# Performance work log

Measured on AMD Instinct MI355X. Metric: run time of the kernel, lower is better.

The kernel has to match this reference:

```python
import jax, jax.numpy as jnp
import numpy as np

N_NODES = 16384
IN_DIM = 256
HEADS = 2
OUT_CH = 256  # per head
SLOPE = 0.2


def _gat_conv(x, edge_index, W, att_src, att_dst, bias):
    """PyG GATConv (v1), heads=2, concat=True, add_self_loops=True."""
    N = x.shape[0]
    loop = jnp.arange(N)
    src = jnp.concatenate([edge_index[0], loop])  # message sources j
    dst = jnp.concatenate([edge_index[1], loop])  # message targets i
    h = (x @ W.T).reshape(N, HEADS, OUT_CH)          # [N,H,C]
    a_src = (h * att_src).sum(-1)                    # [N,H]
    a_dst = (h * att_dst).sum(-1)                    # [N,H]
    e = jax.nn.leaky_relu(a_src[src] + a_dst[dst], SLOPE)  # [E,H]
    # segment softmax over incoming edges of each dst node
    m = jax.ops.segment_max(e, dst, num_segments=N)
    e = jnp.exp(e - m[dst])
    s = jax.ops.segment_sum(e, dst, num_segments=N)
    alpha = e / s[dst]                               # [E,H]
    out = jax.ops.segment_sum(alpha[:, :, None] * h[src], dst, num_segments=N)
    return out.reshape(N, HEADS * OUT_CH) + bias


def _safe_cdist(x):
    sq = (x * x).sum(-1)
    d2 = sq[:, None] + sq[None, :] - 2.0 * (x @ x.T)
    d2 = jnp.maximum(d2, 0.0)
    d = jnp.sqrt(jnp.where(d2 > 0, d2, 1.0))
    return jnp.where(d2 > 0, d, 0.0)


def _linear_init(k, out_f, in_f):
    b = 1.0 / np.sqrt(in_f)
    k1, k2 = jax.random.split(k)
    W = jax.random.uniform(k1, (out_f, in_f), minval=-b, maxval=b, dtype=jnp.float32)
    bias = jax.random.uniform(k2, (out_f,), minval=-b, maxval=b, dtype=jnp.float32)
    return W, bias


def setup_inputs() -> dict:
    key = jax.random.key(0)
    ks = jax.random.split(key, 12)
    x = jax.random.normal(ks[0], (N_NODES, IN_DIM), dtype=jnp.float32)
    edge_index = jax.random.randint(ks[1], (2, 524288), 0, N_NODES, dtype=jnp.int64)
    g = 1.0 / np.sqrt(IN_DIM)
    conv_W = jax.random.normal(ks[2], (HEADS * OUT_CH, IN_DIM), dtype=jnp.float32) * g
    att_src = jax.random.normal(ks[3], (HEADS, OUT_CH), dtype=jnp.float32) * g
    att_dst = jax.random.normal(ks[4], (HEADS, OUT_CH), dtype=jnp.float32) * g
    conv_b = jnp.zeros((HEADS * OUT_CH,), dtype=jnp.float32)
    Wa, ba = _linear_init(ks[5], 256, 512)
    W1, b1 = _linear_init(ks[6], 128, 256)
    W2, b2 = _linear_init(ks[7], 64, 128)
    W3, b3 = _linear_init(ks[8], 32, 64)
    W4, b4 = _linear_init(ks[9], 3, 32)
    return {"x": x, "edge_index": edge_index, "conv_W": conv_W,
            "att_src": att_src, "att_dst": att_dst, "conv_b": conv_b,
            "Wa": Wa, "ba": ba, "W1": W1, "b1": b1, "W2": W2, "b2": b2,
            "W3": W3, "b3": b3, "W4": W4, "b4": b4}


def reference(x, edge_index, conv_W, att_src, att_dst, conv_b,
              Wa, ba, W1, b1, W2, b2, W3, b3, W4, b4):
    h = _gat_conv(x, edge_index, conv_W, att_src, att_dst, conv_b)
    h = jax.nn.relu(h)                      # dropout = identity (eval)
    h = jax.nn.relu(h @ Wa.T + ba)
    h = jax.nn.relu(h @ W1.T + b1)
    h = jax.nn.relu(h @ W2.T + b2)
    h = jax.nn.relu(h @ W3.T + b3)
    h = h @ W4.T + b4                        # [N,3]
    return _safe_cdist(h)                    # [N,N]
```

## Files before the change

### kernel.cpp

```cpp
#include <hip/hip_runtime.h>
#include <hip/hip_bf16.h>
#include <math.h>

#define N_NODES 16384
#define E_EDGES 524288
#define E_TOT   (E_EDGES + N_NODES)
#define HDIM    512
#define SLOPE   0.2f

__global__ void detect_kernel(const void* __restrict__ ei, int* __restrict__ flag) {
    int t = threadIdx.x;
    int v = ((const int*)ei)[2 * t + 1];
    unsigned long long b = __ballot(v != 0);
    if (t == 0) *flag = (b == 0ULL) ? 1 : 0;
}

__device__ __forceinline__ int edge_val(const void* ei, int idx, int is64) {
    if (is64) return (int)((const long long*)ei)[idx];
    return ((const int*)ei)[idx];
}

__global__ __launch_bounds__(256) void count_kernel(const void* __restrict__ ei,
                                                    const int* __restrict__ flag,
                                                    int* __restrict__ deg) {
    int e = blockIdx.x * 256 + threadIdx.x;
    if (e >= E_TOT) return;
    int is64 = *flag;
    int dst = (e < E_EDGES) ? edge_val(ei, E_EDGES + e, is64) : (e - E_EDGES);
    atomicAdd(&deg[dst], 1);
}

__global__ __launch_bounds__(1024) void scan_kernel(const int* __restrict__ deg,
                                                    int* __restrict__ rowptr,
                                                    int* __restrict__ cursor) {
    __shared__ int ps[1024];
    int tid = threadIdx.x;
    int base = tid * 16;
    int loc[16];
    int s = 0;
#pragma unroll
    for (int i = 0; i < 16; ++i) { loc[i] = deg[base + i]; s += loc[i]; }
    ps[tid] = s;
    __syncthreads();
    for (int off = 1; off < 1024; off <<= 1) {
        int t = (tid >= off) ? ps[tid - off] : 0;
        __syncthreads();
        if (tid >= off) ps[tid] += t;
        __syncthreads();
    }
    int run = ps[tid] - s;
#pragma unroll
    for (int i = 0; i < 16; ++i) {
        rowptr[base + i] = run;
        cursor[base + i] = run;
        run += loc[i];
    }
    if (tid == 1023) rowptr[N_NODES] = run;
}

__global__ __launch_bounds__(256) void fill_kernel(const void* __restrict__ ei,
                                                   const int* __restrict__ flag,
                                                   int* __restrict__ cursor,
                                                   int* __restrict__ col) {
    int e = blockIdx.x * 256 + threadIdx.x;
    if (e >= E_TOT) return;
    int is64 = *flag;
    int src, dst;
    if (e < E_EDGES) {
        src = edge_val(ei, e, is64);
        dst = edge_val(ei, E_EDGES + e, is64);
    } else {
        src = dst = e - E_EDGES;
    }
    int slot = atomicAdd(&cursor[dst], 1);
    col[slot] = src;
}

template <bool RELU, bool BIAS>
__global__ __launch_bounds__(256) void gemm128(const float* __restrict__ A,
                                               const float* __restrict__ B,
                                               const float* __restrict__ bias,
                                               float* __restrict__ C,
                                               int M, int N, int K) {
    __shared__ float As[16][132];
    __shared__ float Bs[16][132];
    int tid = threadIdx.x;
    int tx = tid & 15, ty = tid >> 4;
    int bm0 = blockIdx.y * 128, bn0 = blockIdx.x * 128;

    float acc[8][8];
#pragma unroll
    for (int i = 0; i < 8; ++i)
#pragma unroll
        for (int j = 0; j < 8; ++j) acc[i][j] = 0.f;

    for (int k0 = 0; k0 < K; k0 += 16) {
        float4 av[2], bv[2];
#pragma unroll
        for (int l = 0; l < 2; ++l) {
            int idx = l * 256 + tid;
            int row = idx >> 2, k4 = idx & 3;
            av[l] = *(const float4*)&A[(size_t)(bm0 + row) * K + k0 + k4 * 4];
            bv[l] = *(const float4*)&B[(size_t)(bn0 + row) * K + k0 + k4 * 4];
        }
        __syncthreads();
#pragma unroll
        for (int l = 0; l < 2; ++l) {
            int idx = l * 256 + tid;
            int row = idx >> 2, k4 = idx & 3;
            As[k4 * 4 + 0][row] = av[l].x;
            As[k4 * 4 + 1][row] = av[l].y;
            As[k4 * 4 + 2][row] = av[l].z;
            As[k4 * 4 + 3][row] = av[l].w;
            Bs[k4 * 4 + 0][row] = bv[l].x;
            Bs[k4 * 4 + 1][row] = bv[l].y;
            Bs[k4 * 4 + 2][row] = bv[l].z;
            Bs[k4 * 4 + 3][row] = bv[l].w;
        }
        __syncthreads();
#pragma unroll
        for (int kk = 0; kk < 16; ++kk) {
            float4 a0 = *(const float4*)&As[kk][ty * 8];
            float4 a1 = *(const float4*)&As[kk][ty * 8 + 4];
            float4 b0 = *(const float4*)&Bs[kk][tx * 8];
            float4 b1 = *(const float4*)&Bs[kk][tx * 8 + 4];
            float a[8] = {a0.x, a0.y, a0.z, a0.w, a1.x, a1.y, a1.z, a1.w};
            float b[8] = {b0.x, b0.y, b0.z, b0.w, b1.x, b1.y, b1.z, b1.w};
#pragma unroll
            for (int i = 0; i < 8; ++i)
#pragma unroll
                for (int j = 0; j < 8; ++j) acc[i][j] = fmaf(a[i], b[j], acc[i][j]);
        }
        __syncthreads();
    }

    float bvv[8];
#pragma unroll
    for (int j = 0; j < 8; ++j) bvv[j] = BIAS ? bias[bn0 + tx * 8 + j] : 0.f;

#pragma unroll
    for (int i = 0; i < 8; ++i) {
        int row = bm0 + ty * 8 + i;
        float v[8];
#pragma unroll
        for (int j = 0; j < 8; ++j) {
            v[j] = acc[i][j] + bvv[j];
            if (RELU) v[j] = fmaxf(v[j], 0.f);
        }
        float* cp = &C[(size_t)row * N + bn0 + tx * 8];
        *(float4*)cp = make_float4(v[0], v[1], v[2], v[3]);
        *(float4*)(cp + 4) = make_float4(v[4], v[5], v[6], v[7]);
    }
}

__global__ __launch_bounds__(256) void attn_kernel(const float* __restrict__ h,
                                                   const float* __restrict__ att_src,
                                                   const float* __restrict__ att_dst,
                                                   float* __restrict__ a_src,
                                                   float* __restrict__ a_dst) {
    int n = blockIdx.x, tid = threadIdx.x;
    float h0 = h[(size_t)n * HDIM + tid];
    float h1 = h[(size_t)n * HDIM + 256 + tid];
    __shared__ float4 red[256];
    red[tid] = make_float4(h0 * att_src[tid], h1 * att_src[256 + tid],
                           h0 * att_dst[tid], h1 * att_dst[256 + tid]);
    __syncthreads();
    for (int off = 128; off > 0; off >>= 1) {
        if (tid < off) {
            float4 o = red[tid + off];
            float4 m = red[tid];
            m.x += o.x; m.y += o.y; m.z += o.z; m.w += o.w;
            red[tid] = m;
        }
        __syncthreads();
    }
    if (tid == 0) {
        float4 r = red[0];
        a_src[2 * n] = r.x; a_src[2 * n + 1] = r.y;
        a_dst[2 * n] = r.z; a_dst[2 * n + 1] = r.w;
    }
}

__device__ __forceinline__ float lrelu(float x) {
    return fmaxf(x, 0.f) + SLOPE * fminf(x, 0.f);
}

__global__ __launch_bounds__(256) void aggregate_kernel(const float* __restrict__ h,
                                                        const float* __restrict__ a_src,
                                                        const float* __restrict__ a_dst,
                                                        const int* __restrict__ rowptr,
                                                        const int* __restrict__ col,
                                                        const float* __restrict__ conv_b,
                                                        float* __restrict__ act0) {
    int n = blockIdx.x, tid = threadIdx.x;
    int rs = rowptr[n], re = rowptr[n + 1];
    float ad0 = a_dst[2 * n], ad1 = a_dst[2 * n + 1];
    __shared__ float r0[256], r1[256];

    float m0 = -1e30f, m1 = -1e30f;
    for (int k = rs + tid; k < re; k += 256) {
        int s = col[k];
        float e0 = lrelu(a_src[2 * s] + ad0);
        float e1 = lrelu(a_src[2 * s + 1] + ad1);
        m0 = fmaxf(m0, e0); m1 = fmaxf(m1, e1);
    }
    r0[tid] = m0; r1[tid] = m1;
    __syncthreads();
    for (int off = 128; off > 0; off >>= 1) {
        if (tid < off) {
            r0[tid] = fmaxf(r0[tid], r0[tid + off]);
            r1[tid] = fmaxf(r1[tid], r1[tid + off]);
        }
        __syncthreads();
    }
    float M0 = r0[0], M1 = r1[0];
    __syncthreads();

    float s0 = 0.f, s1 = 0.f;
    for (int k = rs + tid; k < re; k += 256) {
        int s = col[k];
        float e0 = lrelu(a_src[2 * s] + ad0);
        float e1 = lrelu(a_src[2 * s + 1] + ad1);
        s0 += expf(e0 - M0); s1 += expf(e1 - M1);
    }
    r0[tid] = s0; r1[tid] = s1;
    __syncthreads();
    for (int off = 128; off > 0; off >>= 1) {
        if (tid < off) {
            r0[tid] += r0[tid + off];
            r1[tid] += r1[tid + off];
        }
        __syncthreads();
    }
    float inv0 = 1.f / r0[0], inv1 = 1.f / r1[0];
    __syncthreads();

    __shared__ float al0[256], al1[256];
    __shared__ int sc[256];
    float acc0 = 0.f, acc1 = 0.f;
    for (int base = rs; base < re; base += 256) {
        int len = min(256, re - base);
        if (tid < len) {
            int s = col[base + tid];
            sc[tid] = s;
            float e0 = lrelu(a_src[2 * s] + ad0);
            float e1 = lrelu(a_src[2 * s + 1] + ad1);
            al0[tid] = expf(e0 - M0) * inv0;
            al1[tid] = expf(e1 - M1) * inv1;
        }
        __syncthreads();
        for (int kk = 0; kk < len; ++kk) {
            const float* hr = h + (size_t)sc[kk] * HDIM;
            acc0 = fmaf(al0[kk], hr[tid], acc0);
            acc1 = fmaf(al1[kk], hr[tid + 256], acc1);
        }
        __syncthreads();
    }
    act0[(size_t)n * HDIM + tid] = fmaxf(acc0 + conv_b[tid], 0.f);
    act0[(size_t)n * HDIM + 256 + tid] = fmaxf(acc1 + conv_b[tid + 256], 0.f);
}

__global__ __launch_bounds__(256) void mlp_tail_kernel(const float* __restrict__ act2,
                                                       const float* __restrict__ W2, const float* __restrict__ b2,
                                                       const float* __restrict__ W3, const float* __restrict__ b3,
                                                       const float* __restrict__ W4, const float* __restrict__ b4,
                                                       float* __restrict__ p) {
    __shared__ float w2[64][129];
    __shared__ float w3[32][65];
    __shared__ float w4[3][33];
    __shared__ float bb2[64], bb3[32], bb4[3];
    __shared__ float xb[4][128];
    __shared__ float yb[4][64];
    __shared__ float zb[4][32];
    int tid = threadIdx.x;
    for (int idx = tid; idx < 64 * 128; idx += 256) w2[idx >> 7][idx & 127] = W2[idx];
    for (int idx = tid; idx < 32 * 64; idx += 256) w3[idx >> 6][idx & 63] = W3[idx];
    for (int idx = tid; idx < 96; idx += 256) w4[idx / 32][idx % 32] = W4[idx];
    if (tid < 64) bb2[tid] = b2[tid];
    if (tid < 32) bb3[tid] = b3[tid];
    if (tid < 3) bb4[tid] = b4[tid];
    __syncthreads();

    int n0 = blockIdx.x * 64;
    int nl = tid >> 6, lane = tid & 63;
    for (int g = 0; g < 64; g += 4) {
        for (int l = tid; l < 512; l += 256)
            xb[l >> 7][l & 127] = act2[(size_t)(n0 + g + (l >> 7)) * 128 + (l & 127)];
        __syncthreads();
        float y = bb2[lane];
#pragma unroll 8
        for (int j = 0; j < 128; ++j) y = fmaf(w2[lane][j], xb[nl][j], y);
        yb[nl][lane] = fmaxf(y, 0.f);
        __syncthreads();
        if (lane < 32) {
            float z = bb3[lane];
#pragma unroll 8
            for (int j = 0; j < 64; ++j) z = fmaf(w3[lane][j], yb[nl][j], z);
            zb[nl][lane] = fmaxf(z, 0.f);
        }
        __syncthreads();
        if (lane < 3) {
            float c = bb4[lane];
#pragma unroll
            for (int j = 0; j < 32; ++j) c = fmaf(w4[lane][j], zb[nl][j], c);
            p[(size_t)(n0 + g + nl) * 3 + lane] = c;
        }
        __syncthreads();
    }
}

__global__ __launch_bounds__(256) void cdist_kernel(const float* __restrict__ p,
                                                    float* __restrict__ out) {
    int tid = threadIdx.x;
    int j0 = blockIdx.x * 1024 + tid * 4;
    int i0 = blockIdx.y * 64;
    __shared__ float pi[64][3];
    for (int l = tid; l < 192; l += 256) pi[l / 3][l % 3] = p[i0 * 3 + l];
    float px[4], py[4], pz[4];
#pragma unroll
    for (int q = 0; q < 4; ++q) {
        const float* pp = p + (size_t)(j0 + q) * 3;
        px[q] = pp[0]; py[q] = pp[1]; pz[q] = pp[2];
    }
    __syncthreads();
#pragma unroll 4
    for (int i = 0; i < 64; ++i) {
        float ax = pi[i][0], ay = pi[i][1], az = pi[i][2];
        float o[4];
#pragma unroll
        for (int q = 0; q < 4; ++q) {
            float dx = ax - px[q], dy = ay - py[q], dz = az - pz[q];
            float d2 = fmaf(dx, dx, fmaf(dy, dy, dz * dz));
            o[q] = (d2 > 0.f) ? sqrtf(d2) : 0.f;
        }
        *(float4*)(out + (size_t)(i0 + i) * N_NODES + j0) = make_float4(o[0], o[1], o[2], o[3]);
    }
}

extern "C" void kernel_launch(void* const* d_in, const int* in_sizes, int n_in,
                              void* d_out, int out_size, void* d_ws, size_t ws_size,
                              hipStream_t stream) {
    const float* x       = (const float*)d_in[0];
    const void*  ei      = d_in[1];
    const float* conv_W  = (const float*)d_in[2];
    const float* att_src = (const float*)d_in[3];
    const float* att_dst = (const float*)d_in[4];
    const float* conv_b  = (const float*)d_in[5];
    const float* Wa = (const float*)d_in[6];  const float* ba = (const float*)d_in[7];
    const float* W1 = (const float*)d_in[8];  const float* b1 = (const float*)d_in[9];
    const float* W2 = (const float*)d_in[10]; const float* b2 = (const float*)d_in[11];
    const float* W3 = (const float*)d_in[12]; const float* b3 = (const float*)d_in[13];
    const float* W4 = (const float*)d_in[14]; const float* b4 = (const float*)d_in[15];
    float* out = (float*)d_out;

    float* ws_f  = (float*)d_ws;
    float* h     = ws_f;
    float* act0  = ws_f + (size_t)N_NODES * HDIM;
    float* a_src = act0 + (size_t)N_NODES * HDIM;
    float* a_dst = a_src + N_NODES * 2;
    int* deg     = (int*)(a_dst + N_NODES * 2);
    int* rowptr  = deg + N_NODES;
    int* cursor  = rowptr + N_NODES + 1;
    int* col     = cursor + N_NODES;
    int* flag    = col + E_TOT;
    float* act1  = h;
    float* act2  = h + (size_t)N_NODES * 256;
    float* p3    = act2 + (size_t)N_NODES * 128;

    hipMemsetAsync(deg, 0, N_NODES * sizeof(int), stream);
    detect_kernel<<<1, 64, 0, stream>>>(ei, flag);

    gemm128<false, false><<<dim3(4, 128), 256, 0, stream>>>(x, conv_W, nullptr, h,
                                                            N_NODES, 512, 256);
    attn_kernel<<<N_NODES, 256, 0, stream>>>(h, att_src, att_dst, a_src, a_dst);

    count_kernel<<<E_TOT / 256, 256, 0, stream>>>(ei, flag, deg);
    scan_kernel<<<1, 1024, 0, stream>>>(deg, rowptr, cursor);
    fill_kernel<<<E_TOT / 256, 256, 0, stream>>>(ei, flag, cursor, col);

    aggregate_kernel<<<N_NODES, 256, 0, stream>>>(h, a_src, a_dst, rowptr, col,
                                                  conv_b, act0);

    gemm128<true, true><<<dim3(2, 128), 256, 0, stream>>>(act0, Wa, ba, act1,
                                                          N_NODES, 256, 512);
    gemm128<true, true><<<dim3(1, 128), 256, 0, stream>>>(act1, W1, b1, act2,
                                                          N_NODES, 128, 256);
    mlp_tail_kernel<<<N_NODES / 64, 256, 0, stream>>>(act2, W2, b2, W3, b3, W4, b4, p3);

    cdist_kernel<<<dim3(16, 256), 256, 0, stream>>>(p3, out);
}
```

Before: 1.642 ms.

## Replace FP32 SIMT GEMMs with split-bf16 MFMA GEMMs via hi/lo operand expansion

Each FP32 GEMM operand is split into bf16 high and low parts and laid out as a K-tripled matrix. The A side is stored as [hi, hi, lo] and the B side as [hi, lo, hi], so one bf16 MFMA GEMM over 3K computes hi*hi + hi*lo + lo*hi, which approximates FP32 accuracy. The new GEMM uses global_load_lds direct-to-LDS copies, XOR-swizzled LDS tiles and 16x16x32 bf16 MFMA instructions. This adds split kernels and extra memory traffic for the expanded operands, and the workspace layout is reorganised so act1 and act2 no longer alias h.

```diff
diff --git a/kernel.cpp b/kernel.cpp
--- a/kernel.cpp
+++ b/kernel.cpp
@@ -1,12 +1,28 @@
 #include <hip/hip_runtime.h>
-#include <hip/hip_bf16.h>
 #include <math.h>
+#include <stdint.h>
 
 #define N_NODES 16384
 #define E_EDGES 524288
 #define E_TOT   (E_EDGES + N_NODES)
 #define HDIM    512
 #define SLOPE   0.2f
+
+typedef unsigned short ushort_t;
+typedef __attribute__((ext_vector_type(8))) short short8v;
+typedef __attribute__((ext_vector_type(4))) float f32x4;
+
+__device__ __forceinline__ unsigned short f2bf(float f) {
+    unsigned u = __float_as_uint(f);
+    return (unsigned short)((u + 0x7fffu + ((u >> 16) & 1u)) >> 16);
+}
+__device__ __forceinline__ float bf2f(unsigned short s) {
+    return __uint_as_float(((unsigned)s) << 16);
+}
+
+#define GLOAD_LDS16(G, L)                                                               \
+    __builtin_amdgcn_global_load_lds((const __attribute__((address_space(1))) unsigned int*)(G), \
+                                     (__attribute__((address_space(3))) unsigned int*)(L), 16, 0, 0)
 
 __global__ void detect_kernel(const void* __restrict__ ei, int* __restrict__ flag) {
     int t = threadIdx.x;
@@ -76,80 +92,121 @@
     col[slot] = src;
 }
 
-template <bool RELU, bool BIAS>
-__global__ __launch_bounds__(256) void gemm128(const float* __restrict__ A,
-                                               const float* __restrict__ B,
-                                               const float* __restrict__ bias,
-                                               float* __restrict__ C,
-                                               int M, int N, int K) {
-    __shared__ float As[16][132];
-    __shared__ float Bs[16][132];
-    int tid = threadIdx.x;
-    int tx = tid & 15, ty = tid >> 4;
-    int bm0 = blockIdx.y * 128, bn0 = blockIdx.x * 128;
-
-    float acc[8][8];
-#pragma unroll
-    for (int i = 0; i < 8; ++i)
-#pragma unroll
-        for (int j = 0; j < 8; ++j) acc[i][j] = 0.f;
-
-    for (int k0 = 0; k0 < K; k0 += 16) {
-        float4 av[2], bv[2];
-#pragma unroll
-        for (int l = 0; l < 2; ++l) {
-            int idx = l * 256 + tid;
-            int row = idx >> 2, k4 = idx & 3;
-            av[l] = *(const float4*)&A[(size_t)(bm0 + row) * K + k0 + k4 * 4];
-            bv[l] = *(const float4*)&B[(size_t)(bn0 + row) * K + k0 + k4 * 4];
-        }
-        __syncthreads();
-#pragma unroll
-        for (int l = 0; l < 2; ++l) {
-            int idx = l * 256 + tid;
-            int row = idx >> 2, k4 = idx & 3;
-            As[k4 * 4 + 0][row] = av[l].x;
-            As[k4 * 4 + 1][row] = av[l].y;
-            As[k4 * 4 + 2][row] = av[l].z;
-            As[k4 * 4 + 3][row] = av[l].w;
-            Bs[k4 * 4 + 0][row] = bv[l].x;
-            Bs[k4 * 4 + 1][row] = bv[l].y;
-            Bs[k4 * 4 + 2][row] = bv[l].z;
-            Bs[k4 * 4 + 3][row] = bv[l].w;
-        }
-        __syncthreads();
-#pragma unroll
-        for (int kk = 0; kk < 16; ++kk) {
-            float4 a0 = *(const float4*)&As[kk][ty * 8];
-            float4 a1 = *(const float4*)&As[kk][ty * 8 + 4];
-            float4 b0 = *(const float4*)&Bs[kk][tx * 8];
-            float4 b1 = *(const float4*)&Bs[kk][tx * 8 + 4];
-            float a[8] = {a0.x, a0.y, a0.z, a0.w, a1.x, a1.y, a1.z, a1.w};
-            float b[8] = {b0.x, b0.y, b0.z, b0.w, b1.x, b1.y, b1.z, b1.w};
-#pragma unroll
-            for (int i = 0; i < 8; ++i)
-#pragma unroll
-                for (int j = 0; j < 8; ++j) acc[i][j] = fmaf(a[i], b[j], acc[i][j]);
-        }
-        __syncthreads();
-    }
-
-    float bvv[8];
-#pragma unroll
-    for (int j = 0; j < 8; ++j) bvv[j] = BIAS ? bias[bn0 + tx * 8 + j] : 0.f;
-
-#pragma unroll
-    for (int i = 0; i < 8; ++i) {
-        int row = bm0 + ty * 8 + i;
-        float v[8];
-#pragma unroll
-        for (int j = 0; j < 8; ++j) {
-            v[j] = acc[i][j] + bvv[j];
-            if (RELU) v[j] = fmaxf(v[j], 0.f);
-        }
-        float* cp = &C[(size_t)row * N + bn0 + tx * 8];
-        *(float4*)cp = make_float4(v[0], v[1], v[2], v[3]);
-        *(float4*)(cp + 4) = make_float4(v[4], v[5], v[6], v[7]);
+template <bool BSTYLE>
+__global__ __launch_bounds__(256) void split3_kernel(const float* __restrict__ src,
+                                                     ushort_t* __restrict__ dst,
+                                                     int kshift) {
+    int idx = (blockIdx.x * 256 + threadIdx.x) * 4;
+    int K = 1 << kshift;
+    int row = idx >> kshift, c = idx & (K - 1);
+    float4 v = *(const float4*)&src[idx];
+    float f[4] = {v.x, v.y, v.z, v.w};
+    ushort_t h4[4], l4[4];
+#pragma unroll
+    for (int q = 0; q < 4; ++q) {
+        ushort_t hb = f2bf(f[q]);
+        float r = f[q] - bf2f(hb);
+        h4[q] = hb;
+        l4[q] = f2bf(r);
+    }
+    size_t b = (size_t)row * (3 * (size_t)K) + c;
+    *(ushort4*)&dst[b] = make_ushort4(h4[0], h4[1], h4[2], h4[3]);
+    size_t off_hi2 = BSTYLE ? (size_t)(2 * K) : (size_t)K;
+    size_t off_lo  = BSTYLE ? (size_t)K : (size_t)(2 * K);
+    *(ushort4*)&dst[b + off_hi2] = make_ushort4(h4[0], h4[1], h4[2], h4[3]);
+    *(ushort4*)&dst[b + off_lo]  = make_ushort4(l4[0], l4[1], l4[2], l4[3]);
+}
+
+template <int BN, bool RELU, bool BIAS>
+__global__ __launch_bounds__(256) void mfma_gemm(const ushort_t* __restrict__ A,
+                                                 const ushort_t* __restrict__ B,
+                                                 const float* __restrict__ bias,
+                                                 float* __restrict__ C,
+                                                 int M, int N, int K) {
+    constexpr int BM = 128, BK = 64;
+    constexpr int ASLOTS = BM * BK / (256 * 8);
+    constexpr int BSLOTS = BN * BK / (256 * 8);
+    constexpr int BNF = BN / 32;
+    __shared__ ushort_t As[BM * BK];
+    __shared__ ushort_t Bs[BN * BK];
+
+    int t = threadIdx.x;
+    int bm0 = blockIdx.y * BM, bn0 = blockIdx.x * BN;
+
+    size_t gA[ASLOTS]; int lA[ASLOTS];
+#pragma unroll
+    for (int s = 0; s < ASLOTS; ++s) {
+        int lin = s * 256 + t;
+        int row = lin >> 3, cs = (lin & 7) << 3;
+        int lcol = cs ^ ((row & 7) << 3);
+        gA[s] = (size_t)(bm0 + row) * K + lcol;
+        lA[s] = (s * 256 + (t & ~63)) * 8;
+    }
+    size_t gB[BSLOTS]; int lB[BSLOTS];
+#pragma unroll
+    for (int s = 0; s < BSLOTS; ++s) {
+        int lin = s * 256 + t;
+        int row = lin >> 3, cs = (lin & 7) << 3;
+        int lcol = cs ^ ((row & 7) << 3);
+        gB[s] = (size_t)(bn0 + row) * K + lcol;
+        lB[s] = (s * 256 + (t & ~63)) * 8;
+    }
+
+    int l = t & 63, w = t >> 6;
+    int wm = w >> 1, wn = w & 1;
+    int lr = l & 15, lk = l >> 4;
+
+    f32x4 acc[4][BNF];
+#pragma unroll
+    for (int m = 0; m < 4; ++m)
+#pragma unroll
+        for (int n = 0; n < BNF; ++n) acc[m][n] = (f32x4){0.f, 0.f, 0.f, 0.f};
+
+    for (int k0 = 0; k0 < K; k0 += BK) {
+#pragma unroll
+        for (int s = 0; s < ASLOTS; ++s) GLOAD_LDS16(A + gA[s] + k0, As + lA[s]);
+#pragma unroll
+        for (int s = 0; s < BSLOTS; ++s) GLOAD_LDS16(B + gB[s] + k0, Bs + lB[s]);
+        __syncthreads();
+#pragma unroll
+        for (int ks = 0; ks < 2; ++ks) {
+            short8v af[4], bfr[BNF];
+#pragma unroll
+            for (int m = 0; m < 4; ++m) {
+                int row = wm * 64 + m * 16 + lr;
+                int c = (ks * 32 + lk * 8) ^ ((row & 7) << 3);
+                af[m] = *(const short8v*)&As[row * 64 + c];
+            }
+#pragma unroll
+            for (int n = 0; n < BNF; ++n) {
+                int row = wn * (BN / 2) + n * 16 + lr;
+                int c = (ks * 32 + lk * 8) ^ ((row & 7) << 3);
+                bfr[n] = *(const short8v*)&Bs[row * 64 + c];
+            }
+#pragma unroll
+            for (int m = 0; m < 4; ++m)
+#pragma unroll
+                for (int n = 0; n < BNF; ++n)
+                    acc[m][n] = __builtin_amdgcn_mfma_f32_16x16x32_bf16(af[m], bfr[n],
+                                                                        acc[m][n], 0, 0, 0);
+        }
+        __syncthreads();
+    }
+
+#pragma unroll
+    for (int m = 0; m < 4; ++m) {
+        int row0 = bm0 + wm * 64 + m * 16 + lk * 4;
+#pragma unroll
+        for (int n = 0; n < BNF; ++n) {
+            int cix = bn0 + wn * (BN / 2) + n * 16 + lr;
+            float bv = BIAS ? bias[cix] : 0.f;
+#pragma unroll
+            for (int r = 0; r < 4; ++r) {
+                float v = acc[m][n][r] + bv;
+                if (RELU) v = fmaxf(v, 0.f);
+                C[(size_t)(row0 + r) * N + cix] = v;
+            }
+        }
     }
 }
 
@@ -284,8 +341,8 @@
     int n0 = blockIdx.x * 64;
     int nl = tid >> 6, lane = tid & 63;
     for (int g = 0; g < 64; g += 4) {
-        for (int l = tid; l < 512; l += 256)
-            xb[l >> 7][l & 127] = act2[(size_t)(n0 + g + (l >> 7)) * 128 + (l & 127)];
+        for (int lx = tid; lx < 512; lx += 256)
+            xb[lx >> 7][lx & 127] = act2[(size_t)(n0 + g + (lx >> 7)) * 128 + (lx & 127)];
         __syncthreads();
         float y = bb2[lane];
 #pragma unroll 8
@@ -315,7 +372,7 @@
     int j0 = blockIdx.x * 1024 + tid * 4;
     int i0 = blockIdx.y * 64;
     __shared__ float pi[64][3];
-    for (int l = tid; l < 192; l += 256) pi[l / 3][l % 3] = p[i0 * 3 + l];
+    for (int lx = tid; lx < 192; lx += 256) pi[lx / 3][lx % 3] = p[i0 * 3 + lx];
     float px[4], py[4], pz[4];
 #pragma unroll
     for (int q = 0; q < 4; ++q) {
@@ -355,36 +412,53 @@
 
     float* ws_f  = (float*)d_ws;
     float* h     = ws_f;
-    float* act0  = ws_f + (size_t)N_NODES * HDIM;
-    float* a_src = act0 + (size_t)N_NODES * HDIM;
+    float* act0  = h     + (size_t)N_NODES * HDIM;
+    float* act1  = act0  + (size_t)N_NODES * HDIM;
+    float* act2  = act1  + (size_t)N_NODES * 256;
+    float* p3    = act2  + (size_t)N_NODES * 128;
+    float* a_src = p3    + (size_t)N_NODES * 4;
     float* a_dst = a_src + N_NODES * 2;
     int* deg     = (int*)(a_dst + N_NODES * 2);
     int* rowptr  = deg + N_NODES;
     int* cursor  = rowptr + N_NODES + 1;
-    int* col     = cursor + N_NODES;
-    int* flag    = col + E_TOT;
-    float* act1  = h;
-    float* act2  = h + (size_t)N_NODES * 256;
-    float* p3    = act2 + (size_t)N_NODES * 128;
+    int* colx    = cursor + N_NODES;
+    int* flag    = colx + E_TOT;
+    uintptr_t up = ((uintptr_t)(flag + 1) + 255) & ~(uintptr_t)255;
+    ushort_t* x2  = (ushort_t*)up;
+    ushort_t* a02 = x2  + (size_t)N_NODES * 768;
+    ushort_t* a12 = a02 + (size_t)N_NODES * 1536;
+    ushort_t* cw2 = a12 + (size_t)N_NODES * 768;
+    ushort_t* wa2 = cw2 + (size_t)512 * 768;
+    ushort_t* w12 = wa2 + (size_t)256 * 1536;
 
     hipMemsetAsync(deg, 0, N_NODES * sizeof(int), stream);
     detect_kernel<<<1, 64, 0, stream>>>(ei, flag);
 
-    gemm128<false, false><<<dim3(4, 128), 256, 0, stream>>>(x, conv_W, nullptr, h,
-                                                            N_NODES, 512, 256);
+    split3_kernel<false><<<N_NODES * 256 / 1024, 256, 0, stream>>>(x, x2, 8);
+    split3_kernel<true><<<512 * 256 / 1024, 256, 0, stream>>>(conv_W, cw2, 8);
+    split3_kernel<true><<<256 * 512 / 1024, 256, 0, stream>>>(Wa, wa2, 9);
+    split3_kernel<true><<<128 * 256 / 1024, 256, 0, stream>>>(W1, w12, 8);
+
+    mfma_gemm<128, false, false><<<dim3(4, 128), 256, 0, stream>>>(
+        x2, cw2, nullptr, h, N_NODES, 512, 768);
+
     attn_kernel<<<N_NODES, 256, 0, stream>>>(h, att_src, att_dst, a_src, a_dst);
 
     count_kernel<<<E_TOT / 256, 256, 0, stream>>>(ei, flag, deg);
     scan_kernel<<<1, 1024, 0, stream>>>(deg, rowptr, cursor);
-    fill_kernel<<<E_TOT / 256, 256, 0, stream>>>(ei, flag, cursor, col);
-
-    aggregate_kernel<<<N_NODES, 256, 0, stream>>>(h, a_src, a_dst, rowptr, col,
+    fill_kernel<<<E_TOT / 256, 256, 0, stream>>>(ei, flag, cursor, colx);
+
+    aggregate_kernel<<<N_NODES, 256, 0, stream>>>(h, a_src, a_dst, rowptr, colx,
                                                   conv_b, act0);
 
-    gemm128<true, true><<<dim3(2, 128), 256, 0, stream>>>(act0, Wa, ba, act1,
-                                                          N_NODES, 256, 512);
-    gemm128<true, true><<<dim3(1, 128), 256, 0, stream>>>(act1, W1, b1, act2,
-                                                          N_NODES, 128, 256);
+    split3_kernel<false><<<N_NODES * 512 / 1024, 256, 0, stream>>>(act0, a02, 9);
+    mfma_gemm<128, true, true><<<dim3(2, 128), 256, 0, stream>>>(
+        a02, wa2, ba, act1, N_NODES, 256, 1536);
+
+    split3_kernel<false><<<N_NODES * 256 / 1024, 256, 0, stream>>>(act1, a12, 8);
+    mfma_gemm<64, true, true><<<dim3(2, 128), 256, 0, stream>>>(
+        a12, w12, b1, act2, N_NODES, 128, 768);
+
     mlp_tail_kernel<<<N_NODES / 64, 256, 0, stream>>>(act2, W2, b2, W3, b3, W4, b4, p3);
 
     cdist_kernel<<<dim3(16, 256), 256, 0, stream>>>(p3, out);
```

Measured after the change: 1.598 ms. -2.6%, faster.
